# Kernel optimization log

Measured on AMD Instinct MI355X. Metric: run time of the kernel, lower is better.

The kernel has to match this reference:

```python
import jax, jax.numpy as jnp
import numpy as np

N_GRAPHS = 8192
HIDDEN = 256
N_NODES = 500000


def setup_inputs() -> dict:
    key = jax.random.key(0)
    k1, k2, k3, k4, k5 = jax.random.split(key, 5)
    x = jax.random.normal(k1, (N_NODES, HIDDEN), dtype=jnp.float32)
    batch = jnp.sort(jax.random.randint(k2, (N_NODES,), 0, N_GRAPHS, dtype=jnp.int32))
    # attention MLP params: Linear(H,H) -> tanh -> Linear(H,1)
    s1 = 1.0 / np.sqrt(HIDDEN)
    W1 = jax.random.uniform(k3, (HIDDEN, HIDDEN), minval=-s1, maxval=s1, dtype=jnp.float32)
    b1 = jnp.zeros((HIDDEN,), dtype=jnp.float32)
    W2 = jax.random.uniform(k4, (HIDDEN, 1), minval=-s1, maxval=s1, dtype=jnp.float32)
    b2 = jnp.zeros((1,), dtype=jnp.float32)
    return {"x": x, "batch": batch, "W1": W1, "b1": b1, "W2": W2, "b2": b2}


def reference(x, batch, W1, b1, W2, b2):
    # attention logits: [N, 1]
    h = jnp.tanh(x @ W1 + b1)
    attn_logits = h @ W2 + b2  # [N, 1]
    e = jnp.exp(attn_logits)   # faithful: no max-subtraction in original
    # segment-sum of exp per graph, gathered back per node
    denom = jax.ops.segment_sum(e, batch, num_segments=N_GRAPHS)  # [G, 1]
    attn_weights = e / (denom[batch] + 1e-8)  # [N, 1]
    weighted_x = x * attn_weights             # [N, H]
    graph_embeddings = jax.ops.segment_sum(weighted_x, batch, num_segments=N_GRAPHS)  # [G, H]
    return graph_embeddings
```

## Files before the change

kernel.cpp:

```cpp
#include <hip/hip_runtime.h>

#define N_NODES  500000
#define HIDDEN   256
#define N_GRAPHS 8192
#define NTILES   (N_NODES / 32)
#define NWIN     (N_NODES / 16)
#define PROW     260

typedef float f32x4 __attribute__((ext_vector_type(4)));
typedef short s16x8 __attribute__((ext_vector_type(8)));

__device__ __forceinline__ unsigned short f2bf(float f) {
    unsigned int u = __float_as_uint(f);
    u += 0x7fffu + ((u >> 16) & 1u);
    return (unsigned short)(u >> 16);
}

__global__ void prep_w1_kernel(const float* __restrict__ W1,
                               unsigned short* __restrict__ w1pack) {
    int tid  = blockIdx.x * 256 + threadIdx.x;
    int lane = tid & 63;
    int slot = tid >> 6;
    int wv   = slot >> 5;
    int kt   = (slot >> 2) & 7;
    int ntp  = slot & 3;
    int nt   = wv * 4 + ntp;
    int krow = kt * 32 + ((lane >> 4) & 3) * 8;
    int col  = nt * 16 + (lane & 15);
    unsigned short tmp[8];
#pragma unroll
    for (int j = 0; j < 8; ++j)
        tmp[j] = f2bf(W1[(size_t)(krow + j) * 256 + col]);
    *(uint4*)(w1pack + (size_t)tid * 8) = *(const uint4*)tmp;
}

__global__ void offsets_kernel(const int* __restrict__ batch,
                               int* __restrict__ offsEnd) {
    int g = blockIdx.x * 256 + threadIdx.x;
    if (g >= N_GRAPHS) return;
    int lo = 0, hi = N_NODES;
    while (lo < hi) {
        int mid = (lo + hi) >> 1;
        if (batch[mid] < g + 1) lo = mid + 1; else hi = mid;
    }
    offsEnd[g] = lo;
}

__launch_bounds__(256, 4)
__global__ void fused_kernel(const float* __restrict__ x,
                             const int*   __restrict__ batch,
                             const float* __restrict__ b1,
                             const float* __restrict__ W2,
                             const float* __restrict__ b2,
                             const unsigned short* __restrict__ w1pack,
                             float* __restrict__ preW,
                             float* __restrict__ sufW,
                             float* __restrict__ out) {
    __shared__ unsigned short xbf[32 * 256];
    __shared__ float plds[128];

    const int tid  = threadIdx.x;
    const int wave = tid >> 6;
    const int lane = tid & 63;
    const int cl   = lane & 15;
    const int kgrp = lane >> 4;
    const int base = blockIdx.x * 32;

#pragma unroll
    for (int i = 0; i < 4; ++i) {
        int v   = tid + i * 256;
        int row = v >> 5;
        int cu  = v & 31;
        const float* p = x + (size_t)(base + row) * HIDDEN + cu * 8;
        f32x4 a = *(const f32x4*)p;
        f32x4 c = *(const f32x4*)(p + 4);
        s16x8 w;
        w[0] = (short)f2bf(a[0]); w[1] = (short)f2bf(a[1]);
        w[2] = (short)f2bf(a[2]); w[3] = (short)f2bf(a[3]);
        w[4] = (short)f2bf(c[0]); w[5] = (short)f2bf(c[1]);
        w[6] = (short)f2bf(c[2]); w[7] = (short)f2bf(c[3]);
        *(s16x8*)(xbf + (size_t)(row * 32 + (cu ^ (row & 7))) * 8) = w;
    }

    float b1c[4], w2c[4];
#pragma unroll
    for (int ntp = 0; ntp < 4; ++ntp) {
        int nt = wave * 4 + ntp;
        b1c[ntp] = b1[nt * 16 + cl];
        w2c[ntp] = W2[nt * 16 + cl];
    }
    const float b2v = b2[0];
    __syncthreads();

    float sj[2][4];
#pragma unroll
    for (int rt = 0; rt < 2; ++rt)
#pragma unroll
        for (int j = 0; j < 4; ++j) sj[rt][j] = 0.f;

#pragma unroll
    for (int pass = 0; pass < 2; ++pass) {
        f32x4 acc[2][2];
#pragma unroll
        for (int rt = 0; rt < 2; ++rt)
#pragma unroll
            for (int p = 0; p < 2; ++p)
                acc[rt][p] = (f32x4){0.f, 0.f, 0.f, 0.f};

#pragma unroll
        for (int kt = 0; kt < 8; ++kt) {
            s16x8 bf[2];
#pragma unroll
            for (int p = 0; p < 2; ++p)
                bf[p] = *(const s16x8*)(w1pack +
                    ((size_t)(((wave * 8 + kt) * 4 + pass * 2 + p) * 64 + lane) << 3));
#pragma unroll
            for (int rt = 0; rt < 2; ++rt) {
                int row = rt * 16 + cl;
                int cu  = kt * 4 + kgrp;
                s16x8 af = *(const s16x8*)(xbf +
                    (size_t)(row * 32 + (cu ^ (row & 7))) * 8);
#pragma unroll
                for (int p = 0; p < 2; ++p)
                    acc[rt][p] = __builtin_amdgcn_mfma_f32_16x16x32_bf16(
                        af, bf[p], acc[rt][p], 0, 0, 0);
            }
        }
#pragma unroll
        for (int rt = 0; rt < 2; ++rt)
#pragma unroll
            for (int p = 0; p < 2; ++p) {
                float bb = b1c[pass * 2 + p];
                float ww = w2c[pass * 2 + p];
#pragma unroll
                for (int j = 0; j < 4; ++j) {
                    float h = acc[rt][p][j] + bb;
                    h = fminf(fmaxf(h, -15.f), 15.f);
                    float e2 = __expf(2.f * h);
                    float th = (e2 - 1.f) * __builtin_amdgcn_rcpf(e2 + 1.f);
                    sj[rt][j] += th * ww;
                }
            }
    }

#pragma unroll
    for (int m = 1; m < 16; m <<= 1)
#pragma unroll
        for (int rt = 0; rt < 2; ++rt)
#pragma unroll
            for (int j = 0; j < 4; ++j)
                sj[rt][j] += __shfl_xor(sj[rt][j], m, 64);
    if (cl == 0) {
#pragma unroll
        for (int rt = 0; rt < 2; ++rt)
#pragma unroll
            for (int j = 0; j < 4; ++j)
                plds[wave * 32 + rt * 16 + kgrp * 4 + j] = sj[rt][j];
    }
    __syncthreads();

    if (wave < 2) {
        const int ws  = base + wave * 16;
        const int wid = blockIdx.x * 2 + wave;
        int rr = wave * 16 + cl;
        float logit = plds[rr] + plds[32 + rr] + plds[64 + rr] + plds[96 + rr] + b2v;
        float el = __expf(logit);

        int bval = batch[ws + cl];
        const int gfirst = __shfl(bval, 0, 64);
        const int glast  = __shfl(bval, 15, 64);
        const bool eb = (ws > 0) && (batch[ws - 1] == gfirst);
        const bool ef = (ws + 16 < N_NODES) && (batch[ws + 16] == glast);

        f32x4 accv = {0.f, 0.f, 0.f, 0.f};
        float accden = 0.f;
        int gcur = gfirst, sl = 0;
#pragma unroll
        for (int r = 0; r < 16; ++r) {
            int   g  = __shfl(bval, r, 64);
            float er = __shfl(el, r, 64);
            if (g != gcur) {
                bool sb = (sl == 0) && eb;
                if (!sb) {
                    float d = accden + 1e-8f;
                    f32x4 res;
                    res[0] = accv[0] / d; res[1] = accv[1] / d;
                    res[2] = accv[2] / d; res[3] = accv[3] / d;
                    *(f32x4*)(out + (size_t)gcur * HIDDEN + lane * 4) = res;
                } else {
                    *(f32x4*)(preW + (size_t)wid * PROW + lane * 4) = accv;
                    if (lane == 0) preW[(size_t)wid * PROW + 256] = accden;
                }
                accv = (f32x4){0.f, 0.f, 0.f, 0.f};
                accden = 0.f;
                gcur = g; sl = r;
            }
            f32x4 xv = *(const f32x4*)(x + (size_t)(ws + r) * HIDDEN + lane * 4);
            accv += er * xv;
            accden += er;
        }
        {
            bool sb = (sl == 0) && eb;
            if (!sb && !ef) {
                float d = accden + 1e-8f;
                f32x4 res;
                res[0] = accv[0] / d; res[1] = accv[1] / d;
                res[2] = accv[2] / d; res[3] = accv[3] / d;
                *(f32x4*)(out + (size_t)gcur * HIDDEN + lane * 4) = res;
            } else if (!sb && sl > 0) {
                *(f32x4*)(sufW + (size_t)wid * PROW + lane * 4) = accv;
                if (lane == 0) sufW[(size_t)wid * PROW + 256] = accden;
            } else {
                *(f32x4*)(preW + (size_t)wid * PROW + lane * 4) = accv;
                if (lane == 0) preW[(size_t)wid * PROW + 256] = accden;
            }
        }
    }
}

__launch_bounds__(256)
__global__ void combine_kernel(const float* __restrict__ preW,
                               const float* __restrict__ sufW,
                               const int* __restrict__ offsEnd,
                               float* __restrict__ out) {
    const int g    = blockIdx.x * 4 + (threadIdx.x >> 6);
    const int lane = threadIdx.x & 63;
    if (g >= N_GRAPHS) return;
    const int s = (g == 0) ? 0 : offsEnd[g - 1];
    const int e = offsEnd[g];
    if (e == s) {
        *(f32x4*)(out + (size_t)g * HIDDEN + lane * 4) = (f32x4){0.f, 0.f, 0.f, 0.f};
        return;
    }
    const int w0 = s >> 4, w1 = (e - 1) >> 4;
    if (w0 == w1) return;

    const float* row = (s > (w0 << 4)) ? sufW + (size_t)w0 * PROW
                                       : preW + (size_t)w0 * PROW;
    f32x4 acc = *(const f32x4*)(row + lane * 4);
    float den = row[256];
    for (int w = w0 + 1; w <= w1; ++w) {
        const float* pr = preW + (size_t)w * PROW;
        acc += *(const f32x4*)(pr + lane * 4);
        den += pr[256];
    }
    float d = den + 1e-8f;
    f32x4 res;
    res[0] = acc[0] / d; res[1] = acc[1] / d;
    res[2] = acc[2] / d; res[3] = acc[3] / d;
    *(f32x4*)(out + (size_t)g * HIDDEN + lane * 4) = res;
}

extern "C" void kernel_launch(void* const* d_in, const int* in_sizes, int n_in,
                              void* d_out, int out_size, void* d_ws, size_t ws_size,
                              hipStream_t stream) {
    const float* x     = (const float*)d_in[0];
    const int*   batch = (const int*)d_in[1];
    const float* W1    = (const float*)d_in[2];
    const float* b1    = (const float*)d_in[3];
    const float* W2    = (const float*)d_in[4];
    const float* b2    = (const float*)d_in[5];
    float* out = (float*)d_out;

    unsigned short* w1pack = (unsigned short*)d_ws;
    int*   offsEnd = (int*)((char*)d_ws + 131072);
    float* preW    = (float*)((char*)d_ws + 163840);
    float* sufW    = (float*)((char*)d_ws + 163840 + (size_t)NWIN * PROW * 4);

    prep_w1_kernel<<<32, 256, 0, stream>>>(W1, w1pack);
    offsets_kernel<<<32, 256, 0, stream>>>(batch, offsEnd);

    fused_kernel<<<NTILES, 256, 0, stream>>>(x, batch, b1, W2, b2, w1pack,
                                             preW, sufW, out);
    combine_kernel<<<(N_GRAPHS + 3) / 4, 256, 0, stream>>>(preW, sufW, offsEnd, out);
}
```

Measured before the change: 221.8 us.

## Make fused kernel persistent with async global-to-LDS prefetch of next tile

```diff
diff --git a/kernel.cpp b/kernel.cpp
--- a/kernel.cpp
+++ b/kernel.cpp
@@ -6,9 +6,13 @@
 #define NTILES   (N_NODES / 32)
 #define NWIN     (N_NODES / 16)
 #define PROW     260
+#define NB       768
 
 typedef float f32x4 __attribute__((ext_vector_type(4)));
 typedef short s16x8 __attribute__((ext_vector_type(8)));
+
+typedef __attribute__((address_space(1))) const void gv_t;
+typedef __attribute__((address_space(3))) void       lv_t;
 
 __device__ __forceinline__ unsigned short f2bf(float f) {
     unsigned int u = __float_as_uint(f);
@@ -46,7 +50,7 @@
     offsEnd[g] = lo;
 }
 
-__launch_bounds__(256, 4)
+__launch_bounds__(256, 3)
 __global__ void fused_kernel(const float* __restrict__ x,
                              const int*   __restrict__ batch,
                              const float* __restrict__ b1,
@@ -56,7 +60,8 @@
                              float* __restrict__ preW,
                              float* __restrict__ sufW,
                              float* __restrict__ out) {
-    __shared__ unsigned short xbf[32 * 256];
+    __shared__ float bufA[32 * 256];
+    __shared__ unsigned short bufB[32 * 256];
     __shared__ float plds[128];
 
     const int tid  = threadIdx.x;
@@ -64,23 +69,6 @@
     const int lane = tid & 63;
     const int cl   = lane & 15;
     const int kgrp = lane >> 4;
-    const int base = blockIdx.x * 32;
-
-#pragma unroll
-    for (int i = 0; i < 4; ++i) {
-        int v   = tid + i * 256;
-        int row = v >> 5;
-        int cu  = v & 31;
-        const float* p = x + (size_t)(base + row) * HIDDEN + cu * 8;
-        f32x4 a = *(const f32x4*)p;
-        f32x4 c = *(const f32x4*)(p + 4);
-        s16x8 w;
-        w[0] = (short)f2bf(a[0]); w[1] = (short)f2bf(a[1]);
-        w[2] = (short)f2bf(a[2]); w[3] = (short)f2bf(a[3]);
-        w[4] = (short)f2bf(c[0]); w[5] = (short)f2bf(c[1]);
-        w[6] = (short)f2bf(c[2]); w[7] = (short)f2bf(c[3]);
-        *(s16x8*)(xbf + (size_t)(row * 32 + (cu ^ (row & 7))) * 8) = w;
-    }
 
     float b1c[4], w2c[4];
 #pragma unroll
@@ -90,129 +78,178 @@
         w2c[ntp] = W2[nt * 16 + cl];
     }
     const float b2v = b2[0];
-    __syncthreads();
-
-    float sj[2][4];
-#pragma unroll
-    for (int rt = 0; rt < 2; ++rt)
-#pragma unroll
-        for (int j = 0; j < 4; ++j) sj[rt][j] = 0.f;
-
-#pragma unroll
-    for (int pass = 0; pass < 2; ++pass) {
-        f32x4 acc[2][2];
+
+    {
+        int t0 = blockIdx.x;
+        if (t0 < NTILES) {
+#pragma unroll
+            for (int i = 0; i < 8; ++i) {
+                int row = wave * 8 + i;
+                const float* src = x + (size_t)(t0 * 32 + row) * HIDDEN + lane * 4;
+                __builtin_amdgcn_global_load_lds((gv_t*)src,
+                                                 (lv_t*)(bufA + row * 256), 16, 0, 0);
+            }
+        }
+    }
+
+    for (int t = blockIdx.x; t < NTILES; t += NB) {
+        __syncthreads();
+
+#pragma unroll
+        for (int i = 0; i < 4; ++i) {
+            int v   = tid + i * 256;
+            int row = v >> 5;
+            int cu  = v & 31;
+            f32x4 a = *(const f32x4*)(bufA + row * 256 + cu * 8);
+            f32x4 c = *(const f32x4*)(bufA + row * 256 + cu * 8 + 4);
+            s16x8 w;
+            w[0] = (short)f2bf(a[0]); w[1] = (short)f2bf(a[1]);
+            w[2] = (short)f2bf(a[2]); w[3] = (short)f2bf(a[3]);
+            w[4] = (short)f2bf(c[0]); w[5] = (short)f2bf(c[1]);
+            w[6] = (short)f2bf(c[2]); w[7] = (short)f2bf(c[3]);
+            *(s16x8*)(bufB + (size_t)(row * 32 + (cu ^ (row & 7))) * 8) = w;
+        }
+        __syncthreads();
+
+        if (t + NB < NTILES) {
+#pragma unroll
+            for (int i = 0; i < 8; ++i) {
+                int row = wave * 8 + i;
+                const float* src = x + (size_t)((t + NB) * 32 + row) * HIDDEN + lane * 4;
+                __builtin_amdgcn_global_load_lds((gv_t*)src,
+                                                 (lv_t*)(bufA + row * 256), 16, 0, 0);
+            }
+        }
+
+        const int base = t * 32;
+        const int ws   = base + (wave & 1) * 16;
+        int bval  = batch[ws + cl];
+        int bprev = (ws > 0) ? batch[ws - 1] : -1;
+        int bnext = (ws + 16 < N_NODES) ? batch[ws + 16] : -1;
+
+        float sj[2][4];
 #pragma unroll
         for (int rt = 0; rt < 2; ++rt)
 #pragma unroll
-            for (int p = 0; p < 2; ++p)
-                acc[rt][p] = (f32x4){0.f, 0.f, 0.f, 0.f};
-
-#pragma unroll
-        for (int kt = 0; kt < 8; ++kt) {
-            s16x8 bf[2];
-#pragma unroll
-            for (int p = 0; p < 2; ++p)
-                bf[p] = *(const s16x8*)(w1pack +
-                    ((size_t)(((wave * 8 + kt) * 4 + pass * 2 + p) * 64 + lane) << 3));
-#pragma unroll
-            for (int rt = 0; rt < 2; ++rt) {
-                int row = rt * 16 + cl;
-                int cu  = kt * 4 + kgrp;
-                s16x8 af = *(const s16x8*)(xbf +
-                    (size_t)(row * 32 + (cu ^ (row & 7))) * 8);
+            for (int j = 0; j < 4; ++j) sj[rt][j] = 0.f;
+
+#pragma unroll
+        for (int pass = 0; pass < 2; ++pass) {
+            f32x4 acc[2][2];
+#pragma unroll
+            for (int rt = 0; rt < 2; ++rt)
 #pragma unroll
                 for (int p = 0; p < 2; ++p)
-                    acc[rt][p] = __builtin_amdgcn_mfma_f32_16x16x32_bf16(
-                        af, bf[p], acc[rt][p], 0, 0, 0);
-            }
-        }
-#pragma unroll
-        for (int rt = 0; rt < 2; ++rt)
-#pragma unroll
-            for (int p = 0; p < 2; ++p) {
-                float bb = b1c[pass * 2 + p];
-                float ww = w2c[pass * 2 + p];
-#pragma unroll
-                for (int j = 0; j < 4; ++j) {
-                    float h = acc[rt][p][j] + bb;
-                    h = fminf(fmaxf(h, -15.f), 15.f);
-                    float e2 = __expf(2.f * h);
-                    float th = (e2 - 1.f) * __builtin_amdgcn_rcpf(e2 + 1.f);
-                    sj[rt][j] += th * ww;
+                    acc[rt][p] = (f32x4){0.f, 0.f, 0.f, 0.f};
+
+#pragma unroll
+            for (int kt = 0; kt < 8; ++kt) {
+                s16x8 bf[2];
+#pragma unroll
+                for (int p = 0; p < 2; ++p)
+                    bf[p] = *(const s16x8*)(w1pack +
+                        ((size_t)(((wave * 8 + kt) * 4 + pass * 2 + p) * 64 + lane) << 3));
+#pragma unroll
+                for (int rt = 0; rt < 2; ++rt) {
+                    int row = rt * 16 + cl;
+                    int cu  = kt * 4 + kgrp;
+                    s16x8 af = *(const s16x8*)(bufB +
+                        (size_t)(row * 32 + (cu ^ (row & 7))) * 8);
+#pragma unroll
+                    for (int p = 0; p < 2; ++p)
+                        acc[rt][p] = __builtin_amdgcn_mfma_f32_16x16x32_bf16(
+                            af, bf[p], acc[rt][p], 0, 0, 0);
                 }
             }
-    }
-
-#pragma unroll
-    for (int m = 1; m < 16; m <<= 1)
-#pragma unroll
-        for (int rt = 0; rt < 2; ++rt)
-#pragma unroll
-            for (int j = 0; j < 4; ++j)
-                sj[rt][j] += __shfl_xor(sj[rt][j], m, 64);
-    if (cl == 0) {
-#pragma unroll
-        for (int rt = 0; rt < 2; ++rt)
-#pragma unroll
-            for (int j = 0; j < 4; ++j)
-                plds[wave * 32 + rt * 16 + kgrp * 4 + j] = sj[rt][j];
-    }
-    __syncthreads();
-
-    if (wave < 2) {
-        const int ws  = base + wave * 16;
-        const int wid = blockIdx.x * 2 + wave;
-        int rr = wave * 16 + cl;
-        float logit = plds[rr] + plds[32 + rr] + plds[64 + rr] + plds[96 + rr] + b2v;
-        float el = __expf(logit);
-
-        int bval = batch[ws + cl];
-        const int gfirst = __shfl(bval, 0, 64);
-        const int glast  = __shfl(bval, 15, 64);
-        const bool eb = (ws > 0) && (batch[ws - 1] == gfirst);
-        const bool ef = (ws + 16 < N_NODES) && (batch[ws + 16] == glast);
-
-        f32x4 accv = {0.f, 0.f, 0.f, 0.f};
-        float accden = 0.f;
-        int gcur = gfirst, sl = 0;
-#pragma unroll
-        for (int r = 0; r < 16; ++r) {
-            int   g  = __shfl(bval, r, 64);
-            float er = __shfl(el, r, 64);
-            if (g != gcur) {
+#pragma unroll
+            for (int rt = 0; rt < 2; ++rt)
+#pragma unroll
+                for (int p = 0; p < 2; ++p) {
+                    float bb = b1c[pass * 2 + p];
+                    float ww = w2c[pass * 2 + p];
+#pragma unroll
+                    for (int j = 0; j < 4; ++j) {
+                        float h = acc[rt][p][j] + bb;
+                        h = fminf(fmaxf(h, -15.f), 15.f);
+                        float e2 = __expf(2.f * h);
+                        float th = (e2 - 1.f) * __builtin_amdgcn_rcpf(e2 + 1.f);
+                        sj[rt][j] += th * ww;
+                    }
+                }
+        }
+
+#pragma unroll
+        for (int m = 1; m < 16; m <<= 1)
+#pragma unroll
+            for (int rt = 0; rt < 2; ++rt)
+#pragma unroll
+                for (int j = 0; j < 4; ++j)
+                    sj[rt][j] += __shfl_xor(sj[rt][j], m, 64);
+        if (cl == 0) {
+#pragma unroll
+            for (int rt = 0; rt < 2; ++rt)
+#pragma unroll
+                for (int j = 0; j < 4; ++j)
+                    plds[wave * 32 + rt * 16 + kgrp * 4 + j] = sj[rt][j];
+        }
+
+        asm volatile("s_waitcnt lgkmcnt(0)" ::: "memory");
+        __builtin_amdgcn_s_barrier();
+        __builtin_amdgcn_sched_barrier(0);
+
+        if (wave < 2) {
+            const int wid = t * 2 + wave;
+            int rr = wave * 16 + cl;
+            float logit = plds[rr] + plds[32 + rr] + plds[64 + rr] + plds[96 + rr] + b2v;
+            float el = __expf(logit);
+
+            const int gfirst = __shfl(bval, 0, 64);
+            const int glast  = __shfl(bval, 15, 64);
+            const bool eb = (bprev == gfirst);
+            const bool ef = (bnext == glast);
+
+            f32x4 accv = {0.f, 0.f, 0.f, 0.f};
+            float accden = 0.f;
+            int gcur = gfirst, sl = 0;
+#pragma unroll
+            for (int r = 0; r < 16; ++r) {
+                int   g  = __shfl(bval, r, 64);
+                float er = __shfl(el, r, 64);
+                if (g != gcur) {
+                    bool sb = (sl == 0) && eb;
+                    if (!sb) {
+                        float d = accden + 1e-8f;
+                        f32x4 res;
+                        res[0] = accv[0] / d; res[1] = accv[1] / d;
+                        res[2] = accv[2] / d; res[3] = accv[3] / d;
+                        *(f32x4*)(out + (size_t)gcur * HIDDEN + lane * 4) = res;
+                    } else {
+                        *(f32x4*)(preW + (size_t)wid * PROW + lane * 4) = accv;
+                        if (lane == 0) preW[(size_t)wid * PROW + 256] = accden;
+                    }
+                    accv = (f32x4){0.f, 0.f, 0.f, 0.f};
+                    accden = 0.f;
+                    gcur = g; sl = r;
+                }
+                f32x4 xv = *(const f32x4*)(x + (size_t)(ws + r) * HIDDEN + lane * 4);
+                accv += er * xv;
+                accden += er;
+            }
+            {
                 bool sb = (sl == 0) && eb;
-                if (!sb) {
+                if (!sb && !ef) {
                     float d = accden + 1e-8f;
                     f32x4 res;
                     res[0] = accv[0] / d; res[1] = accv[1] / d;
                     res[2] = accv[2] / d; res[3] = accv[3] / d;
                     *(f32x4*)(out + (size_t)gcur * HIDDEN + lane * 4) = res;
+                } else if (!sb && sl > 0) {
+                    *(f32x4*)(sufW + (size_t)wid * PROW + lane * 4) = accv;
+                    if (lane == 0) sufW[(size_t)wid * PROW + 256] = accden;
                 } else {
                     *(f32x4*)(preW + (size_t)wid * PROW + lane * 4) = accv;
                     if (lane == 0) preW[(size_t)wid * PROW + 256] = accden;
                 }
-                accv = (f32x4){0.f, 0.f, 0.f, 0.f};
-                accden = 0.f;
-                gcur = g; sl = r;
-            }
-            f32x4 xv = *(const f32x4*)(x + (size_t)(ws + r) * HIDDEN + lane * 4);
-            accv += er * xv;
-            accden += er;
-        }
-        {
-            bool sb = (sl == 0) && eb;
-            if (!sb && !ef) {
-                float d = accden + 1e-8f;
-                f32x4 res;
-                res[0] = accv[0] / d; res[1] = accv[1] / d;
-                res[2] = accv[2] / d; res[3] = accv[3] / d;
-                *(f32x4*)(out + (size_t)gcur * HIDDEN + lane * 4) = res;
-            } else if (!sb && sl > 0) {
-                *(f32x4*)(sufW + (size_t)wid * PROW + lane * 4) = accv;
-                if (lane == 0) sufW[(size_t)wid * PROW + 256] = accden;
-            } else {
-                *(f32x4*)(preW + (size_t)wid * PROW + lane * 4) = accv;
-                if (lane == 0) preW[(size_t)wid * PROW + 256] = accden;
             }
         }
     }
@@ -270,7 +307,7 @@
     prep_w1_kernel<<<32, 256, 0, stream>>>(W1, w1pack);
     offsets_kernel<<<32, 256, 0, stream>>>(batch, offsEnd);
 
-    fused_kernel<<<NTILES, 256, 0, stream>>>(x, batch, b1, W2, b2, w1pack,
-                                             preW, sufW, out);
+    fused_kernel<<<NB, 256, 0, stream>>>(x, batch, b1, W2, b2, w1pack,
+                                         preW, sufW, out);
     combine_kernel<<<(N_GRAPHS + 3) / 4, 256, 0, stream>>>(preW, sufW, offsEnd, out);
 }
```

Result: slower. 510.6 us (+130.2%).
